# Kernel tuning notes

Measured on AMD Instinct MI355X. Metric: run time of the kernel, lower is better.

## Reference

```python
import jax, jax.numpy as jnp
import numpy as np

D_MODEL = 1024
NUM_HEADS = 16
D_HEAD = D_MODEL // NUM_HEADS
THETA = 10000.0
B, S = 2, 2048


def setup_inputs() -> dict:
    key = jax.random.key(0)
    ks = jax.random.split(key, 5)
    std = np.sqrt(2.0 / (D_MODEL + D_MODEL))
    x = jax.random.normal(ks[0], (B, S, D_MODEL), dtype=jnp.float32)
    Wq = jax.random.normal(ks[1], (D_MODEL, D_MODEL), dtype=jnp.float32) * std
    Wk = jax.random.normal(ks[2], (D_MODEL, D_MODEL), dtype=jnp.float32) * std
    Wv = jax.random.normal(ks[3], (D_MODEL, D_MODEL), dtype=jnp.float32) * std
    Wo = jax.random.normal(ks[4], (D_MODEL, D_MODEL), dtype=jnp.float32) * std
    token_positions = jnp.arange(S, dtype=jnp.int32)
    return {"x": x, "Wq": Wq, "Wk": Wk, "Wv": Wv, "Wo": Wo,
            "token_positions": token_positions}


def _apply_rope(t, token_positions):
    # t: [B, H, S, d_head]; interleaved (even/odd) RoPE
    dh = t.shape[-1]
    inv_freq = 1.0 / (THETA ** (jnp.arange(0, dh, 2, dtype=jnp.float32) / dh))
    freqs = token_positions.astype(jnp.float32)[:, None] * inv_freq  # [S, dh/2]
    cos = jnp.cos(freqs)  # broadcasts over B, H
    sin = jnp.sin(freqs)
    x1 = t[..., 0::2]
    x2 = t[..., 1::2]
    r1 = x1 * cos - x2 * sin
    r2 = x1 * sin + x2 * cos
    return jnp.stack([r1, r2], axis=-1).reshape(t.shape)


def reference(x, Wq, Wk, Wv, Wo, token_positions):
    b, s, d = x.shape
    h, dh = NUM_HEADS, D_HEAD

    def proj(W):
        y = x @ W.T  # [B, S, D]
        return y.reshape(b, s, h, dh).transpose(0, 2, 1, 3)  # [B, H, S, dh]

    q = _apply_rope(proj(Wq), token_positions)
    k = _apply_rope(proj(Wk), token_positions)
    v = proj(Wv)

    scores = jnp.einsum('bhqd,bhkd->bhqk', q, k) / jnp.sqrt(jnp.float32(dh))
    causal = jnp.tril(jnp.ones((s, s), dtype=bool))
    scores = jnp.where(causal, scores, jnp.float32(-jnp.inf))
    attn = jax.nn.softmax(scores, axis=-1)
    out = jnp.einsum('bhqk,bhkd->bhqd', attn, v)  # [B, H, S, dh]
    out = out.transpose(0, 2, 1, 3).reshape(b, s, d)
    return out @ Wo.T
```

## Files before the change

### kernel.cpp

```cpp
#include <hip/hip_runtime.h>
#include <hip/hip_bf16.h>
#include <math.h>

#define DMODEL 1024
#define NHEAD  16
#define DHEAD  64
#define BATCH  2
#define SEQ    2048
#define MROWS  (BATCH * SEQ)

typedef __attribute__((ext_vector_type(8))) __bf16 bf16x8;
typedef __attribute__((ext_vector_type(4))) float  f32x4;

__device__ __forceinline__ void load16_lds(const ushort* g, ushort* l) {
    __builtin_amdgcn_global_load_lds(
        (const __attribute__((address_space(1))) unsigned int*)g,
        (__attribute__((address_space(3))) unsigned int*)l, 16, 0, 0);
}

__device__ __forceinline__ ushort bf16u(float v) {
    __hip_bfloat16 h = __float2bfloat16(v);
    return *reinterpret_cast<ushort*>(&h);
}

__global__ __launch_bounds__(256)
void cast_f32_bf16(const float* __restrict__ s, ushort* __restrict__ d, int n) {
    const int i = (blockIdx.x * 256 + threadIdx.x) * 8;
    if (i >= n) return;
    const f32x4 a = *reinterpret_cast<const f32x4*>(s + i);
    const f32x4 b = *reinterpret_cast<const f32x4*>(s + i + 4);
    bf16x8 o;
    #pragma unroll
    for (int j = 0; j < 4; j++) { o[j] = (__bf16)a[j]; o[4 + j] = (__bf16)b[j]; }
    *reinterpret_cast<bf16x8*>(d + i) = o;
}

__global__ __launch_bounds__(256)
void cast_w4(const float* __restrict__ w0, const float* __restrict__ w1,
             const float* __restrict__ w2, const float* __restrict__ w3,
             ushort* __restrict__ dst) {
    const float* src = (blockIdx.y == 0) ? w0 : (blockIdx.y == 1) ? w1
                     : (blockIdx.y == 2) ? w2 : w3;
    const int i = (blockIdx.x * 256 + threadIdx.x) * 8;
    const f32x4 a = *reinterpret_cast<const f32x4*>(src + i);
    const f32x4 b = *reinterpret_cast<const f32x4*>(src + i + 4);
    bf16x8 o;
    #pragma unroll
    for (int j = 0; j < 4; j++) { o[j] = (__bf16)a[j]; o[4 + j] = (__bf16)b[j]; }
    *reinterpret_cast<bf16x8*>(dst + (size_t)blockIdx.y * DMODEL * DMODEL + i) = o;
}

__global__ __launch_bounds__(256)
void rope_tab(const int* __restrict__ pos, float2* __restrict__ tab) {
    const int idx = blockIdx.x * 256 + threadIdx.x;
    const int s = idx >> 5;
    const int i = idx & 31;
    const float p = (float)pos[s];
    const float inv = exp2f(-(float)i * 0.41524101186092f);
    float sn, cs;
    sincosf(p * inv, &sn, &cs);
    tab[idx] = make_float2(cs, sn);
}

__global__ __launch_bounds__(256)
void gemm_qkv(const ushort* __restrict__ A, const ushort* __restrict__ B,
              ushort* __restrict__ C, const float2* __restrict__ tab) {
    __shared__ __align__(16) ushort pool[16384];
    ushort* As = pool;
    ushort* Bs = pool + 8192;
    const int tid  = threadIdx.x;
    const int m0   = blockIdx.y * 128;
    const int n0   = blockIdx.x * 128;
    const int lane = tid & 63;
    const int w    = tid >> 6;
    const int l16  = lane & 15;
    const int quad = lane >> 4;
    const int wm   = (w >> 1) * 64;
    const int wn   = (w & 1) * 64;
    const int srow = tid >> 2;
    const int scol = (tid & 3) * 8;

    f32x4 acc[4][4];
    #pragma unroll
    for (int i = 0; i < 4; i++)
        #pragma unroll
        for (int j = 0; j < 4; j++) acc[i][j] = (f32x4){0.f, 0.f, 0.f, 0.f};

    #pragma unroll
    for (int half = 0; half < 2; half++) {
        const int row = srow + half * 64;
        load16_lds(A + (size_t)(m0 + row) * DMODEL + scol, &As[row * 32 + scol]);
        load16_lds(B + (size_t)(n0 + row) * DMODEL + scol, &Bs[row * 32 + scol]);
    }

    for (int t = 0; t < 32; t++) {
        const int bf = t & 1;
        __syncthreads();
        if (t + 1 < 32) {
            const int k0 = (t + 1) * 32;
            const int o  = (bf ^ 1) * 4096;
            #pragma unroll
            for (int half = 0; half < 2; half++) {
                const int row = srow + half * 64;
                load16_lds(A + (size_t)(m0 + row) * DMODEL + k0 + scol,
                           &As[o + row * 32 + scol]);
                load16_lds(B + (size_t)(n0 + row) * DMODEL + k0 + scol,
                           &Bs[o + row * 32 + scol]);
            }
        }
        const int o = bf * 4096;
        bf16x8 af[4], bfr[4];
        #pragma unroll
        for (int s = 0; s < 4; s++)
            af[s] = *reinterpret_cast<const bf16x8*>(
                &As[o + (wm + s * 16 + l16) * 32 + quad * 8]);
        #pragma unroll
        for (int s = 0; s < 4; s++)
            bfr[s] = *reinterpret_cast<const bf16x8*>(
                &Bs[o + (wn + s * 16 + l16) * 32 + quad * 8]);
        #pragma unroll
        for (int i = 0; i < 4; i++)
            #pragma unroll
            for (int j = 0; j < 4; j++)
                acc[i][j] = __builtin_amdgcn_mfma_f32_16x16x32_bf16(
                    af[i], bfr[j], acc[i][j], 0, 0, 0);
    }

    const int nbase  = n0 + wn;
    const int tensor = nbase >> 10;
    const int hh     = (nbase & 1023) >> 6;
    if (tensor < 2) {
        ushort* Dt = C + (size_t)tensor * ((size_t)MROWS * DMODEL);
        #pragma unroll
        for (int i = 0; i < 4; i++)
            #pragma unroll
            for (int r = 0; r < 4; r++) {
                const int m  = m0 + wm + i * 16 + quad * 4 + r;
                const int bb = m >> 11;
                const int ss = m & (SEQ - 1);
                const float2* trow = tab + ss * 32;
                #pragma unroll
                for (int j = 0; j < 4; j++) {
                    const int f = j * 16 + l16;
                    const float2 cs = trow[f >> 1];
                    const float val = acc[i][j][r];
                    const float prt = __shfl_xor(val, 1, 64);
                    const float out = (f & 1) ? (prt * cs.y + val * cs.x)
                                              : (val * cs.x - prt * cs.y);
                    Dt[(((size_t)(bb * NHEAD + hh)) * SEQ + ss) * DHEAD + f] =
                        bf16u(out);
                }
            }
    } else {
        __syncthreads();
        ushort* Tw = pool + w * 4096;
        #pragma unroll
        for (int i = 0; i < 4; i++)
            #pragma unroll
            for (int j = 0; j < 4; j++) {
                const int f = j * 16 + l16;
                #pragma unroll
                for (int r = 0; r < 4; r++) {
                    const int ml = i * 16 + quad * 4 + r;
                    Tw[f * 64 + (ml ^ ((f & 7) << 3))] = bf16u(acc[i][j][r]);
                }
            }
        ushort* Dv = C + 2 * ((size_t)MROWS * DMODEL);
        const int c  = lane & 7;
        const int fb = lane >> 3;
        #pragma unroll
        for (int rr = 0; rr < 8; rr++) {
            const int fl = rr * 8 + fb;
            const uint4 v = *reinterpret_cast<const uint4*>(
                &Tw[fl * 64 + ((c << 3) ^ ((fl & 7) << 3))]);
            *reinterpret_cast<uint4*>(
                &Dv[(size_t)(hh * 64 + fl) * MROWS + m0 + wm + (c << 3)]) = v;
        }
    }
}

__global__ __launch_bounds__(256)
void gemm_out64(const ushort* __restrict__ A, const ushort* __restrict__ B,
                float* __restrict__ C) {
    __shared__ __align__(16) ushort pool[12288];
    ushort* As = pool;
    ushort* Bs = pool + 4096;
    const int tid  = threadIdx.x;
    const int m0   = blockIdx.y * 64;
    const int n0   = blockIdx.x * 128;
    const int lane = tid & 63;
    const int w    = tid >> 6;
    const int l16  = lane & 15;
    const int quad = lane >> 4;
    const int wm   = (w >> 1) * 32;
    const int wn   = (w & 1) * 64;
    const int srow = tid >> 2;
    const int scol = (tid & 3) * 8;

    const int am  = m0 + srow;
    const int abb = am >> 11;
    const int ass = am & (SEQ - 1);
    const size_t abase = ((size_t)(abb * NHEAD)) * SEQ * DHEAD + (size_t)ass * DHEAD;

    f32x4 acc[2][4];
    #pragma unroll
    for (int i = 0; i < 2; i++)
        #pragma unroll
        for (int j = 0; j < 4; j++) acc[i][j] = (f32x4){0.f, 0.f, 0.f, 0.f};

    {
        const int h = scol >> 6, dh = scol & 63;
        load16_lds(A + abase + (size_t)h * SEQ * DHEAD + dh, &As[srow * 32 + scol]);
        #pragma unroll
        for (int half = 0; half < 2; half++) {
            const int row = srow + half * 64;
            load16_lds(B + (size_t)(n0 + row) * DMODEL + scol, &Bs[row * 32 + scol]);
        }
    }

    for (int t = 0; t < 32; t++) {
        const int bf = t & 1;
        __syncthreads();
        if (t + 1 < 32) {
            const int k0 = (t + 1) * 32;
            const int kk = k0 + scol;
            const int h = kk >> 6, dh = kk & 63;
            load16_lds(A + abase + (size_t)h * SEQ * DHEAD + dh,
                       &As[(bf ^ 1) * 2048 + srow * 32 + scol]);
            #pragma unroll
            for (int half = 0; half < 2; half++) {
                const int row = srow + half * 64;
                load16_lds(B + (size_t)(n0 + row) * DMODEL + k0 + scol,
                           &Bs[(bf ^ 1) * 4096 + row * 32 + scol]);
            }
        }
        const int oa = bf * 2048, ob_ = bf * 4096;
        bf16x8 af[2], bfr[4];
        #pragma unroll
        for (int s = 0; s < 2; s++)
            af[s] = *reinterpret_cast<const bf16x8*>(
                &As[oa + (wm + s * 16 + l16) * 32 + quad * 8]);
        #pragma unroll
        for (int s = 0; s < 4; s++)
            bfr[s] = *reinterpret_cast<const bf16x8*>(
                &Bs[ob_ + (wn + s * 16 + l16) * 32 + quad * 8]);
        #pragma unroll
        for (int i = 0; i < 2; i++)
            #pragma unroll
            for (int j = 0; j < 4; j++)
                acc[i][j] = __builtin_amdgcn_mfma_f32_16x16x32_bf16(
                    af[i], bfr[j], acc[i][j], 0, 0, 0);
    }
    #pragma unroll
    for (int i = 0; i < 2; i++)
        #pragma unroll
        for (int r = 0; r < 4; r++) {
            const int m = m0 + wm + i * 16 + quad * 4 + r;
            #pragma unroll
            for (int j = 0; j < 4; j++)
                C[(size_t)m * DMODEL + n0 + wn + j * 16 + l16] = acc[i][j][r];
        }
}

__global__ __launch_bounds__(256)
void attn_mfma6(const ushort* __restrict__ qb, const ushort* __restrict__ kb,
                const ushort* __restrict__ vtg, ushort* __restrict__ ob) {
    __shared__ __align__(16) ushort Ks[2][4096];
    __shared__ __align__(16) ushort Vs[2][4096];
    __shared__ ushort Pb[4][16][72];

    const int bh   = blockIdx.x;
    const int b    = bh >> 4;
    const int h    = bh & 15;
    const int qt   = (gridDim.y - 1) - blockIdx.y;
    const int tid  = threadIdx.x;
    const int w    = tid >> 6;
    const int lane = tid & 63;
    const int l16  = lane & 15;
    const int quad = lane >> 4;
    const size_t base = (size_t)bh * SEQ * DHEAD;

    const int qlo = qt * 64 + w * 16;

    const float SC = 0.125f * 1.44269504088896f;
    bf16x8 qa[2];
    {
        const size_t qo = base + (size_t)(qlo + l16) * DHEAD + quad * 8;
        qa[0] = *reinterpret_cast<const bf16x8*>(qb + qo);
        qa[1] = *reinterpret_cast<const bf16x8*>(qb + qo + 32);
        #pragma unroll
        for (int j = 0; j < 8; j++) {
            qa[0][j] = (__bf16)(SC * (float)qa[0][j]);
            qa[1][j] = (__bf16)(SC * (float)qa[1][j]);
        }
    }

    f32x4 oacc[4];
    #pragma unroll
    for (int s = 0; s < 4; s++) oacc[s] = (f32x4){0.f, 0.f, 0.f, 0.f};
    float l_ = 0.f;

    const int c0 = tid,        r0 = c0 >> 3, g0 = (c0 & 7) ^ (r0 & 7);
    const int c1 = 256 + tid,  r1 = c1 >> 3, g1 = (c1 & 7) ^ (r1 & 7);
    const ushort* kg0 = kb + base + (size_t)r0 * DHEAD + g0 * 8;
    const ushort* kg1 = kb + base + (size_t)r1 * DHEAD + g1 * 8;
    const ushort* vg0 = vtg + (size_t)(h * DHEAD + r0) * MROWS + b * SEQ + g0 * 8;
    const ushort* vg1 = vtg + (size_t)(h * DHEAD + r1) * MROWS + b * SEQ + g1 * 8;

    int koff[2][4];
    #pragma unroll
    for (int half = 0; half < 2; half++)
        #pragma unroll
        for (int sub = 0; sub < 4; sub++)
            koff[half][sub] = (sub * 16 + l16) * 64 +
                              (((half * 4 + quad) ^ (l16 & 7)) * 8);

    load16_lds(kg0, &Ks[0][c0 * 8]);
    load16_lds(kg1, &Ks[0][c1 * 8]);
    load16_lds(vg0, &Vs[0][c0 * 8]);
    load16_lds(vg1, &Vs[0][c1 * 8]);

    const int T = qt + 1;
    for (int t = 0; t < T; t++) {
        const int bf = t & 1;
        __syncthreads();
        if (t + 1 < T) {
            const size_t ko = (size_t)(t + 1) * 64 * DHEAD;
            const int    vo = (t + 1) * 64;
            load16_lds(kg0 + ko, &Ks[bf ^ 1][c0 * 8]);
            load16_lds(kg1 + ko, &Ks[bf ^ 1][c1 * 8]);
            load16_lds(vg0 + vo, &Vs[bf ^ 1][c0 * 8]);
            load16_lds(vg1 + vo, &Vs[bf ^ 1][c1 * 8]);
        }

        const bool diag = (t == qt);
        const int nsub = diag ? (w + 1) : 4;
        const int nhv  = diag ? ((w >> 1) + 1) : 2;

        f32x4 sacc[4];
        #pragma unroll
        for (int s = 0; s < 4; s++) sacc[s] = (f32x4){0.f, 0.f, 0.f, 0.f};
        #pragma unroll
        for (int half = 0; half < 2; half++)
            #pragma unroll
            for (int sub = 0; sub < 4; sub++)
                if (sub < nsub) {
                    const bf16x8 kf = *reinterpret_cast<const bf16x8*>(
                        &Ks[bf][koff[half][sub]]);
                    sacc[sub] = __builtin_amdgcn_mfma_f32_16x16x32_bf16(
                        kf, qa[half], sacc[sub], 0, 0, 0);
                }

        float ev[4][4];
        if (diag) {
            const int thr = qlo + l16 - t * 64;
            #pragma unroll
            for (int sub = 0; sub < 4; sub++)
                #pragma unroll
                for (int r = 0; r < 4; r++) {
                    const float e = (sub * 16 + quad * 4 + r <= thr)
                                        ? exp2f(sacc[sub][r]) : 0.f;
                    ev[sub][r] = e;
                    l_ += e;
                }
        } else {
            #pragma unroll
            for (int sub = 0; sub < 4; sub++)
                #pragma unroll
                for (int r = 0; r < 4; r++) {
                    const float e = exp2f(sacc[sub][r]);
                    ev[sub][r] = e;
                    l_ += e;
                }
        }

        #pragma unroll
        for (int sub = 0; sub < 4; sub++) {
            ushort4 pk;
            pk.x = bf16u(ev[sub][0]); pk.y = bf16u(ev[sub][1]);
            pk.z = bf16u(ev[sub][2]); pk.w = bf16u(ev[sub][3]);
            *reinterpret_cast<ushort4*>(&Pb[w][l16][sub * 16 + quad * 4]) = pk;
        }
        bf16x8 pa[2];
        pa[0] = *reinterpret_cast<const bf16x8*>(&Pb[w][l16][quad * 8]);
        pa[1] = *reinterpret_cast<const bf16x8*>(&Pb[w][l16][32 + quad * 8]);

        #pragma unroll
        for (int hk = 0; hk < 2; hk++) {
            if (hk >= nhv) break;
            #pragma unroll
            for (int sf = 0; sf < 4; sf++) {
                const bf16x8 vf = *reinterpret_cast<const bf16x8*>(
                    &Vs[bf][koff[hk][sf]]);
                oacc[sf] = __builtin_amdgcn_mfma_f32_16x16x32_bf16(
                    pa[hk], vf, oacc[sf], 0, 0, 0);
            }
        }
    }

    l_ += __shfl_xor(l_, 16, 64);
    l_ += __shfl_xor(l_, 32, 64);
    float inv[4];
    #pragma unroll
    for (int r = 0; r < 4; r++) inv[r] = 1.f / __shfl(l_, quad * 4 + r, 64);
    #pragma unroll
    for (int sub = 0; sub < 4; sub++)
        #pragma unroll
        for (int r = 0; r < 4; r++) {
            const int q = qlo + quad * 4 + r;
            ob[base + (size_t)q * DHEAD + sub * 16 + l16] =
                bf16u(oacc[sub][r] * inv[r]);
        }
}

extern "C" void kernel_launch(void* const* d_in, const int* in_sizes, int n_in,
                              void* d_out, int out_size, void* d_ws, size_t ws_size,
                              hipStream_t stream) {
    const float* x  = (const float*)d_in[0];
    const float* Wq = (const float*)d_in[1];
    const float* Wk = (const float*)d_in[2];
    const float* Wv = (const float*)d_in[3];
    const float* Wo = (const float*)d_in[4];
    const int* pos = (const int*)d_in[5];

    const size_t TEN = (size_t)MROWS * DMODEL;
    const size_t WEL = (size_t)DMODEL * DMODEL;
    ushort* xb   = (ushort*)d_ws;
    ushort* Wqkv = xb + TEN;
    ushort* Wob  = Wqkv + 3 * WEL;
    ushort* qb   = Wob + WEL;
    ushort* kb   = qb + TEN;
    ushort* vtb  = kb + TEN;
    ushort* ob   = vtb + TEN;
    float2* tab  = (float2*)(ob + TEN);

    dim3 blk(256);
    rope_tab<<<(SEQ * 32) / 256, blk, 0, stream>>>(pos, tab);
    cast_f32_bf16<<<TEN / (8 * 256), blk, 0, stream>>>(x, xb, (int)TEN);
    dim3 gcw(WEL / (8 * 256), 4);
    cast_w4<<<gcw, blk, 0, stream>>>(Wq, Wk, Wv, Wo, Wqkv);

    dim3 gqkv(3 * DMODEL / 128, MROWS / 128);
    gemm_qkv<<<gqkv, blk, 0, stream>>>(xb, Wqkv, qb, tab);

    dim3 gattn(BATCH * NHEAD, SEQ / 64);
    attn_mfma6<<<gattn, blk, 0, stream>>>(qb, kb, vtb, ob);

    dim3 gout(DMODEL / 128, MROWS / 64);
    gemm_out64<<<gout, blk, 0, stream>>>(ob, Wob, (float*)d_out);
}
```

Baseline: 188.8 us.

## Merge prep kernels into one launch and load K fragments directly from global

Fuses the RoPE table, activation cast and weight cast kernels into a single prep launch that dispatches on block index, removing two kernel launches. In attention, K tiles are no longer staged through double-buffered shared memory; each wave reads its MFMA K fragments straight from global memory into registers, while V keeps the LDS pipeline. This frees LDS and drops the K async copies, but K reads become uncoalesced per-lane global loads issued within the loop with no prefetch, which may expose latency and raise register pressure.

```diff
diff --git a/kernel.cpp b/kernel.cpp
--- a/kernel.cpp
+++ b/kernel.cpp
@@ -24,42 +24,44 @@
 }
 
 __global__ __launch_bounds__(256)
-void cast_f32_bf16(const float* __restrict__ s, ushort* __restrict__ d, int n) {
-    const int i = (blockIdx.x * 256 + threadIdx.x) * 8;
-    if (i >= n) return;
-    const f32x4 a = *reinterpret_cast<const f32x4*>(s + i);
-    const f32x4 b = *reinterpret_cast<const f32x4*>(s + i + 4);
-    bf16x8 o;
-    #pragma unroll
-    for (int j = 0; j < 4; j++) { o[j] = (__bf16)a[j]; o[4 + j] = (__bf16)b[j]; }
-    *reinterpret_cast<bf16x8*>(d + i) = o;
-}
-
-__global__ __launch_bounds__(256)
-void cast_w4(const float* __restrict__ w0, const float* __restrict__ w1,
-             const float* __restrict__ w2, const float* __restrict__ w3,
-             ushort* __restrict__ dst) {
-    const float* src = (blockIdx.y == 0) ? w0 : (blockIdx.y == 1) ? w1
-                     : (blockIdx.y == 2) ? w2 : w3;
-    const int i = (blockIdx.x * 256 + threadIdx.x) * 8;
-    const f32x4 a = *reinterpret_cast<const f32x4*>(src + i);
-    const f32x4 b = *reinterpret_cast<const f32x4*>(src + i + 4);
-    bf16x8 o;
-    #pragma unroll
-    for (int j = 0; j < 4; j++) { o[j] = (__bf16)a[j]; o[4 + j] = (__bf16)b[j]; }
-    *reinterpret_cast<bf16x8*>(dst + (size_t)blockIdx.y * DMODEL * DMODEL + i) = o;
-}
-
-__global__ __launch_bounds__(256)
-void rope_tab(const int* __restrict__ pos, float2* __restrict__ tab) {
-    const int idx = blockIdx.x * 256 + threadIdx.x;
-    const int s = idx >> 5;
-    const int i = idx & 31;
-    const float p = (float)pos[s];
-    const float inv = exp2f(-(float)i * 0.41524101186092f);
-    float sn, cs;
-    sincosf(p * inv, &sn, &cs);
-    tab[idx] = make_float2(cs, sn);
+void prep(const float* __restrict__ x,
+          const float* __restrict__ w0, const float* __restrict__ w1,
+          const float* __restrict__ w2, const float* __restrict__ w3,
+          const int* __restrict__ pos,
+          ushort* __restrict__ xb, ushort* __restrict__ wdst,
+          float2* __restrict__ tab) {
+    const int blk = blockIdx.x;
+    const int tid = threadIdx.x;
+    if (blk < 256) {
+        const int idx = blk * 256 + tid;
+        const int s = idx >> 5;
+        const int i = idx & 31;
+        const float p = (float)pos[s];
+        const float inv = exp2f(-(float)i * 0.41524101186092f);
+        float sn, cs;
+        sincosf(p * inv, &sn, &cs);
+        tab[idx] = make_float2(cs, sn);
+    } else if (blk < 2304) {
+        const int i = ((blk - 256) * 256 + tid) * 8;
+        const f32x4 a = *reinterpret_cast<const f32x4*>(x + i);
+        const f32x4 b = *reinterpret_cast<const f32x4*>(x + i + 4);
+        bf16x8 o;
+        #pragma unroll
+        for (int j = 0; j < 4; j++) { o[j] = (__bf16)a[j]; o[4 + j] = (__bf16)b[j]; }
+        *reinterpret_cast<bf16x8*>(xb + i) = o;
+    } else {
+        const int bi = blk - 2304;
+        const int which = bi >> 9;
+        const float* src = (which == 0) ? w0 : (which == 1) ? w1
+                         : (which == 2) ? w2 : w3;
+        const int i = ((bi & 511) * 256 + tid) * 8;
+        const f32x4 a = *reinterpret_cast<const f32x4*>(src + i);
+        const f32x4 b = *reinterpret_cast<const f32x4*>(src + i + 4);
+        bf16x8 o;
+        #pragma unroll
+        for (int j = 0; j < 4; j++) { o[j] = (__bf16)a[j]; o[4 + j] = (__bf16)b[j]; }
+        *reinterpret_cast<bf16x8*>(wdst + (size_t)which * DMODEL * DMODEL + i) = o;
+    }
 }
 
 __global__ __launch_bounds__(256)
@@ -263,9 +265,8 @@
 }
 
 __global__ __launch_bounds__(256)
-void attn_mfma6(const ushort* __restrict__ qb, const ushort* __restrict__ kb,
+void attn_mfma7(const ushort* __restrict__ qb, const ushort* __restrict__ kb,
                 const ushort* __restrict__ vtg, ushort* __restrict__ ob) {
-    __shared__ __align__(16) ushort Ks[2][4096];
     __shared__ __align__(16) ushort Vs[2][4096];
     __shared__ ushort Pb[4][16][72];
 
@@ -302,21 +303,19 @@
 
     const int c0 = tid,        r0 = c0 >> 3, g0 = (c0 & 7) ^ (r0 & 7);
     const int c1 = 256 + tid,  r1 = c1 >> 3, g1 = (c1 & 7) ^ (r1 & 7);
-    const ushort* kg0 = kb + base + (size_t)r0 * DHEAD + g0 * 8;
-    const ushort* kg1 = kb + base + (size_t)r1 * DHEAD + g1 * 8;
     const ushort* vg0 = vtg + (size_t)(h * DHEAD + r0) * MROWS + b * SEQ + g0 * 8;
     const ushort* vg1 = vtg + (size_t)(h * DHEAD + r1) * MROWS + b * SEQ + g1 * 8;
 
-    int koff[2][4];
+    int voff[2][4];
     #pragma unroll
     for (int half = 0; half < 2; half++)
         #pragma unroll
         for (int sub = 0; sub < 4; sub++)
-            koff[half][sub] = (sub * 16 + l16) * 64 +
+            voff[half][sub] = (sub * 16 + l16) * 64 +
                               (((half * 4 + quad) ^ (l16 & 7)) * 8);
 
-    load16_lds(kg0, &Ks[0][c0 * 8]);
-    load16_lds(kg1, &Ks[0][c1 * 8]);
+    const ushort* kfb = kb + base + (size_t)l16 * DHEAD + quad * 8;
+
     load16_lds(vg0, &Vs[0][c0 * 8]);
     load16_lds(vg1, &Vs[0][c1 * 8]);
 
@@ -325,10 +324,7 @@
         const int bf = t & 1;
         __syncthreads();
         if (t + 1 < T) {
-            const size_t ko = (size_t)(t + 1) * 64 * DHEAD;
-            const int    vo = (t + 1) * 64;
-            load16_lds(kg0 + ko, &Ks[bf ^ 1][c0 * 8]);
-            load16_lds(kg1 + ko, &Ks[bf ^ 1][c1 * 8]);
+            const int vo = (t + 1) * 64;
             load16_lds(vg0 + vo, &Vs[bf ^ 1][c0 * 8]);
             load16_lds(vg1 + vo, &Vs[bf ^ 1][c1 * 8]);
         }
@@ -337,6 +333,15 @@
         const int nsub = diag ? (w + 1) : 4;
         const int nhv  = diag ? ((w >> 1) + 1) : 2;
 
+        bf16x8 kf[2][4];
+        #pragma unroll
+        for (int half = 0; half < 2; half++)
+            #pragma unroll
+            for (int sub = 0; sub < 4; sub++)
+                if (sub < nsub)
+                    kf[half][sub] = *reinterpret_cast<const bf16x8*>(
+                        kfb + (size_t)(t * 64 + sub * 16) * DHEAD + half * 32);
+
         f32x4 sacc[4];
         #pragma unroll
         for (int s = 0; s < 4; s++) sacc[s] = (f32x4){0.f, 0.f, 0.f, 0.f};
@@ -344,12 +349,9 @@
         for (int half = 0; half < 2; half++)
             #pragma unroll
             for (int sub = 0; sub < 4; sub++)
-                if (sub < nsub) {
-                    const bf16x8 kf = *reinterpret_cast<const bf16x8*>(
-                        &Ks[bf][koff[half][sub]]);
+                if (sub < nsub)
                     sacc[sub] = __builtin_amdgcn_mfma_f32_16x16x32_bf16(
-                        kf, qa[half], sacc[sub], 0, 0, 0);
-                }
+                        kf[half][sub], qa[half], sacc[sub], 0, 0, 0);
 
         float ev[4][4];
         if (diag) {
@@ -391,7 +393,7 @@
             #pragma unroll
             for (int sf = 0; sf < 4; sf++) {
                 const bf16x8 vf = *reinterpret_cast<const bf16x8*>(
-                    &Vs[bf][koff[hk][sf]]);
+                    &Vs[bf][voff[hk][sf]]);
                 oacc[sf] = __builtin_amdgcn_mfma_f32_16x16x32_bf16(
                     pa[hk], vf, oacc[sf], 0, 0, 0);
             }
@@ -435,16 +437,13 @@
     float2* tab  = (float2*)(ob + TEN);
 
     dim3 blk(256);
-    rope_tab<<<(SEQ * 32) / 256, blk, 0, stream>>>(pos, tab);
-    cast_f32_bf16<<<TEN / (8 * 256), blk, 0, stream>>>(x, xb, (int)TEN);
-    dim3 gcw(WEL / (8 * 256), 4);
-    cast_w4<<<gcw, blk, 0, stream>>>(Wq, Wk, Wv, Wo, Wqkv);
+    prep<<<4352, blk, 0, stream>>>(x, Wq, Wk, Wv, Wo, pos, xb, Wqkv, tab);
 
     dim3 gqkv(3 * DMODEL / 128, MROWS / 128);
     gemm_qkv<<<gqkv, blk, 0, stream>>>(xb, Wqkv, qb, tab);
 
     dim3 gattn(BATCH * NHEAD, SEQ / 64);
-    attn_mfma6<<<gattn, blk, 0, stream>>>(qb, kb, vtb, ob);
+    attn_mfma7<<<gattn, blk, 0, stream>>>(qb, kb, vtb, ob);
 
     dim3 gout(DMODEL / 128, MROWS / 64);
     gemm_out64<<<gout, blk, 0, stream>>>(ob, Wob, (float*)d_out);
```

Result: slower. 231.6 us (+22.7%).
